# Optimization experiments

Measured on AMD Instinct MI355X. Metric: run time of the kernel, lower is better.

The kernel has to match this reference:

```python
import jax, jax.numpy as jnp
import numpy as np

NEG_SLOPE = 0.2  # PyG GATConv default negative_slope


def _gat_edge_forward(x, edge_index, edge_attr, W, W_edge, att_src, att_dst, att_edge, bias):
    N = x.shape[0]
    H, C = att_src.shape
    src, dst = edge_index[0], edge_index[1]

    # --- add self loops with edge_attr fill_value='mean' (PyG default) ---
    ones = jnp.ones((edge_attr.shape[0],), dtype=x.dtype)
    cnt = jax.ops.segment_sum(ones, dst, num_segments=N)  # [N]
    attr_sum = jax.ops.segment_sum(edge_attr, dst, num_segments=N)  # [N, edge_dim]
    loop_attr = attr_sum / jnp.maximum(cnt, 1.0)[:, None]  # mean, 0 if no in-edges
    loop_idx = jnp.arange(N, dtype=edge_index.dtype)
    src_all = jnp.concatenate([src, loop_idx])
    dst_all = jnp.concatenate([dst, loop_idx])
    attr_all = jnp.concatenate([edge_attr, loop_attr], axis=0)  # [E+N, edge_dim]

    # --- linear projections ---
    x_l = (x @ W).reshape(N, H, C)  # [N,H,C]; GATConv uses same lin for src/dst
    a_src = jnp.einsum('nhc,hc->nh', x_l, att_src)  # [N,H]
    a_dst = jnp.einsum('nhc,hc->nh', x_l, att_dst)  # [N,H]
    e = (attr_all @ W_edge).reshape(-1, H, C)  # [E+N,H,C]
    a_edge = jnp.einsum('ehc,hc->eh', e, att_edge)  # [E+N,H]

    # --- per-edge attention logits + segment softmax over incoming edges ---
    logits = jax.nn.leaky_relu(a_src[src_all] + a_dst[dst_all] + a_edge, NEG_SLOPE)
    m = jax.ops.segment_max(logits, dst_all, num_segments=N)  # [N,H]
    p = jnp.exp(logits - m[dst_all])
    denom = jax.ops.segment_sum(p, dst_all, num_segments=N)  # [N,H]
    alpha = p / denom[dst_all]  # [E+N,H]

    # --- weighted scatter aggregation ---
    msgs = alpha[:, :, None] * x_l[src_all]  # [E+N,H,C]
    out = jax.ops.segment_sum(msgs, dst_all, num_segments=N)  # [N,H,C]
    return out.reshape(N, H * C) + bias  # concat=True -> [N, H*C]


def setup_inputs() -> dict:
    key = jax.random.key(0)
    ks = jax.random.split(key, 8)
    N, E, DIN, EDIM, H, C = 100000, 1600000, 128, 16, 4, 32
    s = 1.0 / np.sqrt(DIN)
    return {
        'x': jax.random.normal(ks[0], (N, DIN), jnp.float32),
        'edge_index': jax.random.randint(ks[1], (2, E), 0, N, jnp.int64),
        'edge_attr': jax.random.normal(ks[2], (E, EDIM), jnp.float32),
        'W': jax.random.normal(ks[3], (DIN, H * C), jnp.float32) * s,
        'W_edge': jax.random.normal(ks[4], (EDIM, H * C), jnp.float32) * (1.0 / np.sqrt(EDIM)),
        'att_src': jax.random.normal(ks[5], (H, C), jnp.float32) * 0.1,
        'att_dst': jax.random.normal(ks[6], (H, C), jnp.float32) * 0.1,
        'att_edge': jax.random.normal(ks[7], (H, C), jnp.float32) * 0.1,
        'bias': jnp.zeros((H * C,), jnp.float32),
    }


def reference(x, edge_index, edge_attr, W, W_edge, att_src, att_dst, att_edge, bias):
    return _gat_edge_forward(x, edge_index, edge_attr, W, W_edge, att_src, att_dst, att_edge, bias)
```

## Files before the change

### kernel.cpp

```cpp
#include <hip/hip_runtime.h>
#include <hip/hip_fp16.h>
#include <math.h>

#define NEG_SLOPE 0.2f
typedef unsigned short ushort_t;
typedef unsigned int uint_t;

__global__ void k_prep(const int* __restrict__ ei, int* __restrict__ is64,
                       int* __restrict__ deg, int N,
                       const float* __restrict__ W_edge, const float* __restrict__ att_edge,
                       float* __restrict__ v_edge) {
  int b = blockIdx.x, t = threadIdx.x;
  if (b == 0) {
    __shared__ int any;
    if (t == 0) any = 0;
    __syncthreads();
    if (ei[2 * t + 1] != 0) atomicOr(&any, 1);
    __syncthreads();
    if (t == 0) *is64 = (any == 0) ? 1 : 0;
  } else if (b == 1) {
    if (t < 64) {
      int h = t >> 4, j = t & 15;
      float s = 0.f;
#pragma unroll
      for (int c = 0; c < 32; ++c) s += W_edge[j * 128 + h * 32 + c] * att_edge[h * 32 + c];
      v_edge[t] = s;
    }
  } else {
    int i = (b - 2) * 256 + t;
    if (i < N) deg[i] = 0;
  }
}

__global__ __launch_bounds__(256) void k1_xl(
    const float* __restrict__ x, const float* __restrict__ W,
    const float* __restrict__ att_src, const float* __restrict__ att_dst,
    ushort_t* __restrict__ x_l_h, float* __restrict__ a_src, float* __restrict__ a_dst, int N) {
  __shared__ float Wc[32 * 128];
  __shared__ float Xc[32 * 64];
  const int t = threadIdx.x;
  const int tcol = t & 31;
  const int trow = t >> 5;
  const int row0 = blockIdx.x * 64;
  const int r = t & 63, kq = t >> 6;
  const float4 aw_s = *(const float4*)&att_src[tcol * 4];
  const float4 aw_d = *(const float4*)&att_dst[tcol * 4];
  float acc[8][4];
#pragma unroll
  for (int i = 0; i < 8; ++i) { acc[i][0] = acc[i][1] = acc[i][2] = acc[i][3] = 0.f; }

  for (int kc = 0; kc < 4; ++kc) {
    float4 wreg[4];
#pragma unroll
    for (int q = 0; q < 4; ++q) wreg[q] = *(const float4*)&W[kc * 4096 + (q * 256 + t) * 4];
    float xs8[8];
    int grow = row0 + r;
    if (grow < N) {
      *(float4*)&xs8[0] = *(const float4*)&x[grow * 128 + kc * 32 + kq * 8];
      *(float4*)&xs8[4] = *(const float4*)&x[grow * 128 + kc * 32 + kq * 8 + 4];
    } else {
#pragma unroll
      for (int q = 0; q < 8; ++q) xs8[q] = 0.f;
    }
    __syncthreads();
#pragma unroll
    for (int q = 0; q < 4; ++q) *(float4*)&Wc[(q * 256 + t) * 4] = wreg[q];
#pragma unroll
    for (int q = 0; q < 8; ++q) Xc[(kq * 8 + q) * 64 + r] = xs8[q];
    __syncthreads();
#pragma unroll
    for (int kk = 0; kk < 32; ++kk) {
      float4 wv = *(const float4*)&Wc[kk * 128 + tcol * 4];
      float xr[8];
      *(float4*)&xr[0] = *(const float4*)&Xc[kk * 64 + trow * 8];
      *(float4*)&xr[4] = *(const float4*)&Xc[kk * 64 + trow * 8 + 4];
#pragma unroll
      for (int ri = 0; ri < 8; ++ri) {
        acc[ri][0] += xr[ri] * wv.x;
        acc[ri][1] += xr[ri] * wv.y;
        acc[ri][2] += xr[ri] * wv.z;
        acc[ri][3] += xr[ri] * wv.w;
      }
    }
  }
#pragma unroll
  for (int ri = 0; ri < 8; ++ri) {
    int grow = row0 + trow * 8 + ri;
    float asp = acc[ri][0] * aw_s.x + acc[ri][1] * aw_s.y + acc[ri][2] * aw_s.z + acc[ri][3] * aw_s.w;
    float adp = acc[ri][0] * aw_d.x + acc[ri][1] * aw_d.y + acc[ri][2] * aw_d.z + acc[ri][3] * aw_d.w;
#pragma unroll
    for (int m = 1; m < 8; m <<= 1) { asp += __shfl_xor(asp, m); adp += __shfl_xor(adp, m); }
    if (grow < N) {
      __half2 h0 = __floats2half2_rn(acc[ri][0], acc[ri][1]);
      __half2 h1 = __floats2half2_rn(acc[ri][2], acc[ri][3]);
      uint2 u; u.x = *(uint_t*)&h0; u.y = *(uint_t*)&h1;
      *(uint2*)&x_l_h[(size_t)grow * 128 + tcol * 4] = u;
      if ((tcol & 7) == 0) {
        a_src[grow * 4 + (tcol >> 3)] = asp;
        a_dst[grow * 4 + (tcol >> 3)] = adp;
      }
    }
  }
}

__global__ void k_hist(const int* __restrict__ ei, const int* __restrict__ is64,
                       int* __restrict__ deg, int* __restrict__ rank, int E) {
  int i = blockIdx.x * blockDim.x + threadIdx.x;
  if (i >= E) return;
  int dst = (*is64) ? ei[2 * (E + i)] : ei[E + i];
  rank[i] = atomicAdd(&deg[dst], 1);
}

__global__ void k_scan1(const int* __restrict__ deg, int* __restrict__ bsum, int N) {
  __shared__ int lds[256];
  int b = blockIdx.x, t = threadIdx.x;
  int base = b * 1024 + t * 4;
  int s = 0;
  if (base + 3 < N) {
    int4 v = *(const int4*)&deg[base];
    s = v.x + v.y + v.z + v.w;
  } else {
    for (int q = 0; q < 4; ++q) if (base + q < N) s += deg[base + q];
  }
  lds[t] = s; __syncthreads();
  for (int st = 128; st > 0; st >>= 1) {
    if (t < st) lds[t] += lds[t + st];
    __syncthreads();
  }
  if (t == 0) bsum[b] = lds[0];
}

__global__ void k_scan2(const int* __restrict__ bsum, int* __restrict__ boff, int NB) {
  __shared__ int lds[256];
  int t = threadIdx.x;
  int v = (t < NB) ? bsum[t] : 0;
  lds[t] = v;
  __syncthreads();
  for (int st = 1; st < 256; st <<= 1) {
    int add = (t >= st) ? lds[t - st] : 0;
    __syncthreads();
    lds[t] += add;
    __syncthreads();
  }
  if (t < NB) boff[t] = lds[t] - v;
}

__global__ void k_scan3(const int* __restrict__ deg, const int* __restrict__ boff,
                        int* __restrict__ offs, int N) {
  __shared__ int lds[256];
  int b = blockIdx.x, t = threadIdx.x;
  int base = b * 1024 + t * 4;
  int v[4]; int s = 0;
#pragma unroll
  for (int q = 0; q < 4; ++q) { v[q] = (base + q < N) ? deg[base + q] : 0; s += v[q]; }
  lds[t] = s;
  __syncthreads();
  for (int st = 1; st < 256; st <<= 1) {
    int add = (t >= st) ? lds[t - st] : 0;
    __syncthreads();
    lds[t] += add;
    __syncthreads();
  }
  int run = boff[b] + lds[t] - s;
#pragma unroll
  for (int q = 0; q < 4; ++q) {
    if (base + q < N) offs[base + q] = run;
    run += v[q];
  }
}

__global__ __launch_bounds__(256) void k_scatter(
    const int* __restrict__ ei, const int* __restrict__ is64,
    const int* __restrict__ rank, const int* __restrict__ offs,
    const float* __restrict__ edge_attr, const float* __restrict__ v_edge,
    int4* __restrict__ rec, int E) {
  __shared__ float ve[64];
  int t = threadIdx.x;
  if (t < 64) ve[t] = v_edge[t];
  __syncthreads();
  int i = blockIdx.x * 256 + t;
  if (i >= E) return;
  int f = *is64;
  int src = f ? ei[2 * i] : ei[i];
  int dst = f ? ei[2 * (E + i)] : ei[E + i];
  float a16[16];
  *(float4*)&a16[0]  = *(const float4*)&edge_attr[(size_t)i * 16];
  *(float4*)&a16[4]  = *(const float4*)&edge_attr[(size_t)i * 16 + 4];
  *(float4*)&a16[8]  = *(const float4*)&edge_attr[(size_t)i * 16 + 8];
  *(float4*)&a16[12] = *(const float4*)&edge_attr[(size_t)i * 16 + 12];
  float ae[4];
#pragma unroll
  for (int h = 0; h < 4; ++h) {
    float s = 0.f;
#pragma unroll
    for (int j = 0; j < 16; ++j) s += a16[j] * ve[h * 16 + j];
    ae[h] = s;
  }
  int pos = offs[dst] + rank[i];
  __half2 e01 = __floats2half2_rn(ae[0], ae[1]);
  __half2 e23 = __floats2half2_rn(ae[2], ae[3]);
  int4 r; r.x = *(int*)&e01; r.y = *(int*)&e23; r.z = src; r.w = 0;
  rec[pos] = r;
}

__global__ __launch_bounds__(256) void k34_agg(
    const int4* __restrict__ rec, const ushort_t* __restrict__ x_l_h,
    const float* __restrict__ a_src, const float* __restrict__ a_dst,
    const int* __restrict__ deg, const int* __restrict__ offs,
    const float* __restrict__ bias, float* __restrict__ out, int N) {
  int lane = threadIdx.x & 63;
  int node = blockIdx.x * 4 + (threadIdx.x >> 6);
  if (node >= N) return;
  int off = offs[node], dg = deg[node];
  int h = lane >> 4;
  float ad = a_dst[(size_t)node * 4 + h];
  const uint_t* xu = (const uint_t*)x_l_h;
  float accx = 0.f, accy = 0.f, den = 0.f, sae = 0.f;
  int i = 0;
  for (; i + 4 <= dg; i += 4) {
    int4 u0 = rec[off + i], u1 = rec[off + i + 1], u2 = rec[off + i + 2], u3 = rec[off + i + 3];
    uint_t v0 = xu[(size_t)u0.z * 64 + lane];
    uint_t v1 = xu[(size_t)u1.z * 64 + lane];
    uint_t v2 = xu[(size_t)u2.z * 64 + lane];
    uint_t v3 = xu[(size_t)u3.z * 64 + lane];
    float s0 = a_src[(size_t)u0.z * 4 + h];
    float s1 = a_src[(size_t)u1.z * 4 + h];
    float s2 = a_src[(size_t)u2.z * 4 + h];
    float s3 = a_src[(size_t)u3.z * 4 + h];
    uint_t w0 = (h & 2) ? (uint_t)u0.y : (uint_t)u0.x;
    uint_t w1 = (h & 2) ? (uint_t)u1.y : (uint_t)u1.x;
    uint_t w2 = (h & 2) ? (uint_t)u2.y : (uint_t)u2.x;
    uint_t w3 = (h & 2) ? (uint_t)u3.y : (uint_t)u3.x;
    float2 q0 = __half22float2(*(const __half2*)&w0);
    float2 q1 = __half22float2(*(const __half2*)&w1);
    float2 q2 = __half22float2(*(const __half2*)&w2);
    float2 q3 = __half22float2(*(const __half2*)&w3);
    float e0 = (h & 1) ? q0.y : q0.x;
    float e1 = (h & 1) ? q1.y : q1.x;
    float e2 = (h & 1) ? q2.y : q2.x;
    float e3 = (h & 1) ? q3.y : q3.x;
    float g0 = s0 + ad + e0; g0 = (g0 >= 0.f) ? g0 : NEG_SLOPE * g0;
    float g1 = s1 + ad + e1; g1 = (g1 >= 0.f) ? g1 : NEG_SLOPE * g1;
    float g2 = s2 + ad + e2; g2 = (g2 >= 0.f) ? g2 : NEG_SLOPE * g2;
    float g3 = s3 + ad + e3; g3 = (g3 >= 0.f) ? g3 : NEG_SLOPE * g3;
    float p0 = __expf(g0), p1 = __expf(g1), p2 = __expf(g2), p3 = __expf(g3);
    den += p0 + p1 + p2 + p3;
    sae += e0 + e1 + e2 + e3;
    float2 f0 = __half22float2(*(const __half2*)&v0);
    float2 f1 = __half22float2(*(const __half2*)&v1);
    float2 f2 = __half22float2(*(const __half2*)&v2);
    float2 f3 = __half22float2(*(const __half2*)&v3);
    accx += p0 * f0.x; accy += p0 * f0.y;
    accx += p1 * f1.x; accy += p1 * f1.y;
    accx += p2 * f2.x; accy += p2 * f2.y;
    accx += p3 * f3.x; accy += p3 * f3.y;
  }
  for (; i < dg; ++i) {
    int4 u = rec[off + i];
    uint_t v = xu[(size_t)u.z * 64 + lane];
    float as = a_src[(size_t)u.z * 4 + h];
    uint_t w = (h & 2) ? (uint_t)u.y : (uint_t)u.x;
    float2 q = __half22float2(*(const __half2*)&w);
    float ae = (h & 1) ? q.y : q.x;
    float g = as + ad + ae; g = (g >= 0.f) ? g : NEG_SLOPE * g;
    float p = __expf(g);
    den += p; sae += ae;
    float2 f = __half22float2(*(const __half2*)&v);
    accx += p * f.x; accy += p * f.y;
  }
  float as_n = a_src[(size_t)node * 4 + h];
  float inv_cnt = 1.f / (float)(dg > 0 ? dg : 1);
  float gl = as_n + ad + sae * inv_cnt;
  gl = (gl >= 0.f) ? gl : NEG_SLOPE * gl;
  float pl = __expf(gl);
  float iv = 1.f / (den + pl);
  uint_t vn = xu[(size_t)node * 64 + lane];
  float2 fn = __half22float2(*(const __half2*)&vn);
  float2 b2 = *(const float2*)&bias[2 * lane];
  float2 o;
  o.x = (accx + pl * fn.x) * iv + b2.x;
  o.y = (accy + pl * fn.y) * iv + b2.y;
  *(float2*)&out[(size_t)node * 128 + 2 * lane] = o;
}

extern "C" void kernel_launch(void* const* d_in, const int* in_sizes, int n_in,
                              void* d_out, int out_size, void* d_ws, size_t ws_size,
                              hipStream_t stream) {
  const float* x        = (const float*)d_in[0];
  const int*   ei       = (const int*)  d_in[1];
  const float* eattr    = (const float*)d_in[2];
  const float* W        = (const float*)d_in[3];
  const float* W_edge   = (const float*)d_in[4];
  const float* att_src  = (const float*)d_in[5];
  const float* att_dst  = (const float*)d_in[6];
  const float* att_edge = (const float*)d_in[7];
  const float* bias     = (const float*)d_in[8];
  float* out = (float*)d_out;
  const int N = in_sizes[0] / 128;
  const int E = in_sizes[1] / 2;
  (void)n_in; (void)out_size; (void)ws_size;

  char* base = (char*)d_ws;
  size_t off = 0;
  auto take = [&](size_t bytes) -> void* {
    void* p = base + off;
    off = (off + bytes + 255) & ~(size_t)255;
    return p;
  };
  ushort_t* x_l_h = (ushort_t*)take((size_t)N * 128 * 2);
  float* a_src    = (float*)take((size_t)N * 4 * 4);
  float* a_dst    = (float*)take((size_t)N * 4 * 4);
  float* v_edge   = (float*)take(64 * 4);
  int4*  rec      = (int4*)take((size_t)E * 16);
  int*   deg      = (int*)take((size_t)N * 4);
  int*   offs     = (int*)take((size_t)N * 4);
  int*   rank     = (int*)take((size_t)E * 4);
  int*   bsum     = (int*)take(256 * 4);
  int*   boff     = (int*)take(256 * 4);
  int*   is64     = (int*)take(4);

  const int NB = (N + 1023) / 1024;
  const int nbh = (E + 255) / 256;

  hipLaunchKernelGGL(k_prep, dim3(2 + (N + 255) / 256), dim3(256), 0, stream,
                     ei, is64, deg, N, W_edge, att_edge, v_edge);
  hipLaunchKernelGGL(k_hist, dim3(nbh), dim3(256), 0, stream, ei, is64, deg, rank, E);
  hipLaunchKernelGGL(k1_xl, dim3((N + 63) / 64), dim3(256), 0, stream,
                     x, W, att_src, att_dst, x_l_h, a_src, a_dst, N);
  hipLaunchKernelGGL(k_scan1, dim3(NB), dim3(256), 0, stream, deg, bsum, N);
  hipLaunchKernelGGL(k_scan2, dim3(1), dim3(256), 0, stream, bsum, boff, NB);
  hipLaunchKernelGGL(k_scan3, dim3(NB), dim3(256), 0, stream, deg, boff, offs, N);
  hipLaunchKernelGGL(k_scatter, dim3(nbh), dim3(256), 0, stream,
                     ei, is64, rank, offs, eattr, v_edge, rec, E);
  hipLaunchKernelGGL(k34_agg, dim3((N + 3) / 4), dim3(256), 0, stream,
                     rec, x_l_h, a_src, a_dst, deg, offs, bias, out, N);
}
```

Baseline: 295.1 us.

## Precompute unnormalized edge attention weights in scatter kernel, store fp8 edge logits

Moves the per-edge logit computation (a_src gather, leaky ReLU, exp) from the aggregation kernel into the scatter kernel. The scatter kernel now writes fp16 exp weights plus fp8-packed edge attention terms into the record, so aggregation skips the random a_src gathers and the exps. Source indices and offsets are made wave-uniform with readfirstlane so the x_l row addresses become scalar. The exp is taken without subtracting the segment max and the edge terms used for the self-loop mean are stored in fp8, which risks overflow and extra rounding error.

```diff
diff --git a/kernel.cpp b/kernel.cpp
--- a/kernel.cpp
+++ b/kernel.cpp
@@ -5,6 +5,46 @@
 #define NEG_SLOPE 0.2f
 typedef unsigned short ushort_t;
 typedef unsigned int uint_t;
+
+#if defined(__has_builtin)
+#if __has_builtin(__builtin_amdgcn_cvt_pk_fp8_f32) && __has_builtin(__builtin_amdgcn_cvt_f32_fp8)
+#define HAVE_FP8_CVT 1
+#endif
+#endif
+
+__device__ __forceinline__ uint_t pack_fp8x4(float a, float b, float c, float d) {
+#ifdef HAVE_FP8_CVT
+  int v = __builtin_amdgcn_cvt_pk_fp8_f32(a, b, 0, false);
+  v = __builtin_amdgcn_cvt_pk_fp8_f32(c, d, v, true);
+  return (uint_t)v;
+#else
+  auto enc = [](float x) -> uint_t {
+    uint_t bb = __float_as_uint(x);
+    uint_t s = (bb >> 24) & 0x80u;
+    int e = (int)((bb >> 23) & 0xffu);
+    uint_t m = (bb >> 20) & 7u;
+    m += (bb >> 19) & 1u;
+    if (m > 7u) { m = 0u; e++; }
+    e = e - 127 + 7;
+    if (e <= 0) return s;
+    if (e > 15) return s | 0x7eu;
+    return s | ((uint_t)e << 3) | m;
+  };
+  return enc(a) | (enc(b) << 8) | (enc(c) << 16) | (enc(d) << 24);
+#endif
+}
+
+__device__ __forceinline__ float unpack_fp8(uint_t w, int shift) {
+#ifdef HAVE_FP8_CVT
+  return __builtin_amdgcn_cvt_f32_fp8((int)(w >> shift), 0);
+#else
+  uint_t b = (w >> shift) & 0xffu;
+  uint_t s = (b & 0x80u) << 24;
+  uint_t em = b & 0x7fu;
+  uint_t f = s | ((em << 20) + (120u << 23));
+  return (em == 0u) ? __uint_as_float(s) : __uint_as_float(f);
+#endif
+}
 
 __global__ void k_prep(const int* __restrict__ ei, int* __restrict__ is64,
                        int* __restrict__ deg, int N,
@@ -173,6 +213,7 @@
     const int* __restrict__ ei, const int* __restrict__ is64,
     const int* __restrict__ rank, const int* __restrict__ offs,
     const float* __restrict__ edge_attr, const float* __restrict__ v_edge,
+    const float* __restrict__ a_src, const float* __restrict__ a_dst,
     int4* __restrict__ rec, int E) {
   __shared__ float ve[64];
   int t = threadIdx.x;
@@ -196,56 +237,62 @@
     for (int j = 0; j < 16; ++j) s += a16[j] * ve[h * 16 + j];
     ae[h] = s;
   }
+  float4 as4 = *(const float4*)&a_src[(size_t)src * 4];
+  float4 ad4 = *(const float4*)&a_dst[(size_t)dst * 4];
+  const float* asp = (const float*)&as4;
+  const float* adp = (const float*)&ad4;
+  float p[4];
+#pragma unroll
+  for (int h = 0; h < 4; ++h) {
+    float g = asp[h] + adp[h] + ae[h];
+    g = fmaxf(g, NEG_SLOPE * g);
+    p[h] = __expf(g);
+  }
+  __half2 p01 = __floats2half2_rn(p[0], p[1]);
+  __half2 p23 = __floats2half2_rn(p[2], p[3]);
+  uint_t aepk = pack_fp8x4(ae[0], ae[1], ae[2], ae[3]);
   int pos = offs[dst] + rank[i];
-  __half2 e01 = __floats2half2_rn(ae[0], ae[1]);
-  __half2 e23 = __floats2half2_rn(ae[2], ae[3]);
-  int4 r; r.x = *(int*)&e01; r.y = *(int*)&e23; r.z = src; r.w = 0;
+  int4 r; r.x = *(int*)&p01; r.y = *(int*)&p23; r.z = src; r.w = (int)aepk;
   rec[pos] = r;
 }
 
 __global__ __launch_bounds__(256) void k34_agg(
-    const int4* __restrict__ rec, const ushort_t* __restrict__ x_l_h,
+    const int4* __restrict__ rec, const uint_t* __restrict__ xu,
     const float* __restrict__ a_src, const float* __restrict__ a_dst,
     const int* __restrict__ deg, const int* __restrict__ offs,
     const float* __restrict__ bias, float* __restrict__ out, int N) {
   int lane = threadIdx.x & 63;
   int node = blockIdx.x * 4 + (threadIdx.x >> 6);
   if (node >= N) return;
-  int off = offs[node], dg = deg[node];
+  int offu = __builtin_amdgcn_readfirstlane(offs[node]);
+  int dgu  = __builtin_amdgcn_readfirstlane(deg[node]);
+  const int4* rp = rec + offu;
   int h = lane >> 4;
-  float ad = a_dst[(size_t)node * 4 + h];
-  const uint_t* xu = (const uint_t*)x_l_h;
+  int hs16 = (h & 1) << 4;
+  int hs8  = h << 3;
   float accx = 0.f, accy = 0.f, den = 0.f, sae = 0.f;
   int i = 0;
-  for (; i + 4 <= dg; i += 4) {
-    int4 u0 = rec[off + i], u1 = rec[off + i + 1], u2 = rec[off + i + 2], u3 = rec[off + i + 3];
-    uint_t v0 = xu[(size_t)u0.z * 64 + lane];
-    uint_t v1 = xu[(size_t)u1.z * 64 + lane];
-    uint_t v2 = xu[(size_t)u2.z * 64 + lane];
-    uint_t v3 = xu[(size_t)u3.z * 64 + lane];
-    float s0 = a_src[(size_t)u0.z * 4 + h];
-    float s1 = a_src[(size_t)u1.z * 4 + h];
-    float s2 = a_src[(size_t)u2.z * 4 + h];
-    float s3 = a_src[(size_t)u3.z * 4 + h];
+  for (; i + 4 <= dgu; i += 4) {
+    int4 u0 = rp[i], u1 = rp[i + 1], u2 = rp[i + 2], u3 = rp[i + 3];
+    int s0 = __builtin_amdgcn_readfirstlane(u0.z);
+    int s1 = __builtin_amdgcn_readfirstlane(u1.z);
+    int s2 = __builtin_amdgcn_readfirstlane(u2.z);
+    int s3 = __builtin_amdgcn_readfirstlane(u3.z);
+    uint_t v0 = xu[((size_t)(uint_t)s0 << 6) + lane];
+    uint_t v1 = xu[((size_t)(uint_t)s1 << 6) + lane];
+    uint_t v2 = xu[((size_t)(uint_t)s2 << 6) + lane];
+    uint_t v3 = xu[((size_t)(uint_t)s3 << 6) + lane];
     uint_t w0 = (h & 2) ? (uint_t)u0.y : (uint_t)u0.x;
     uint_t w1 = (h & 2) ? (uint_t)u1.y : (uint_t)u1.x;
     uint_t w2 = (h & 2) ? (uint_t)u2.y : (uint_t)u2.x;
     uint_t w3 = (h & 2) ? (uint_t)u3.y : (uint_t)u3.x;
-    float2 q0 = __half22float2(*(const __half2*)&w0);
-    float2 q1 = __half22float2(*(const __half2*)&w1);
-    float2 q2 = __half22float2(*(const __half2*)&w2);
-    float2 q3 = __half22float2(*(const __half2*)&w3);
-    float e0 = (h & 1) ? q0.y : q0.x;
-    float e1 = (h & 1) ? q1.y : q1.x;
-    float e2 = (h & 1) ? q2.y : q2.x;
-    float e3 = (h & 1) ? q3.y : q3.x;
-    float g0 = s0 + ad + e0; g0 = (g0 >= 0.f) ? g0 : NEG_SLOPE * g0;
-    float g1 = s1 + ad + e1; g1 = (g1 >= 0.f) ? g1 : NEG_SLOPE * g1;
-    float g2 = s2 + ad + e2; g2 = (g2 >= 0.f) ? g2 : NEG_SLOPE * g2;
-    float g3 = s3 + ad + e3; g3 = (g3 >= 0.f) ? g3 : NEG_SLOPE * g3;
-    float p0 = __expf(g0), p1 = __expf(g1), p2 = __expf(g2), p3 = __expf(g3);
+    float p0 = __half2float(__ushort_as_half((ushort_t)(w0 >> hs16)));
+    float p1 = __half2float(__ushort_as_half((ushort_t)(w1 >> hs16)));
+    float p2 = __half2float(__ushort_as_half((ushort_t)(w2 >> hs16)));
+    float p3 = __half2float(__ushort_as_half((ushort_t)(w3 >> hs16)));
     den += p0 + p1 + p2 + p3;
-    sae += e0 + e1 + e2 + e3;
+    sae += unpack_fp8((uint_t)u0.w, hs8) + unpack_fp8((uint_t)u1.w, hs8)
+         + unpack_fp8((uint_t)u2.w, hs8) + unpack_fp8((uint_t)u3.w, hs8);
     float2 f0 = __half22float2(*(const __half2*)&v0);
     float2 f1 = __half22float2(*(const __half2*)&v1);
     float2 f2 = __half22float2(*(const __half2*)&v2);
@@ -255,26 +302,25 @@
     accx += p2 * f2.x; accy += p2 * f2.y;
     accx += p3 * f3.x; accy += p3 * f3.y;
   }
-  for (; i < dg; ++i) {
-    int4 u = rec[off + i];
-    uint_t v = xu[(size_t)u.z * 64 + lane];
-    float as = a_src[(size_t)u.z * 4 + h];
+  for (; i < dgu; ++i) {
+    int4 u = rp[i];
+    int s = __builtin_amdgcn_readfirstlane(u.z);
+    uint_t v = xu[((size_t)(uint_t)s << 6) + lane];
     uint_t w = (h & 2) ? (uint_t)u.y : (uint_t)u.x;
-    float2 q = __half22float2(*(const __half2*)&w);
-    float ae = (h & 1) ? q.y : q.x;
-    float g = as + ad + ae; g = (g >= 0.f) ? g : NEG_SLOPE * g;
-    float p = __expf(g);
-    den += p; sae += ae;
-    float2 f = __half22float2(*(const __half2*)&v);
-    accx += p * f.x; accy += p * f.y;
-  }
-  float as_n = a_src[(size_t)node * 4 + h];
-  float inv_cnt = 1.f / (float)(dg > 0 ? dg : 1);
-  float gl = as_n + ad + sae * inv_cnt;
-  gl = (gl >= 0.f) ? gl : NEG_SLOPE * gl;
+    float p = __half2float(__ushort_as_half((ushort_t)(w >> hs16)));
+    den += p;
+    sae += unpack_fp8((uint_t)u.w, hs8);
+    float2 fx = __half22float2(*(const __half2*)&v);
+    accx += p * fx.x; accy += p * fx.y;
+  }
+  float ad  = a_dst[(size_t)node * 4 + h];
+  float asn = a_src[(size_t)node * 4 + h];
+  float inv_cnt = 1.f / (float)(dgu > 0 ? dgu : 1);
+  float gl = asn + ad + sae * inv_cnt;
+  gl = fmaxf(gl, NEG_SLOPE * gl);
   float pl = __expf(gl);
   float iv = 1.f / (den + pl);
-  uint_t vn = xu[(size_t)node * 64 + lane];
+  uint_t vn = xu[((size_t)(uint_t)node << 6) + lane];
   float2 fn = __half22float2(*(const __half2*)&vn);
   float2 b2 = *(const float2*)&bias[2 * lane];
   float2 o;
@@ -331,7 +377,7 @@
   hipLaunchKernelGGL(k_scan2, dim3(1), dim3(256), 0, stream, bsum, boff, NB);
   hipLaunchKernelGGL(k_scan3, dim3(NB), dim3(256), 0, stream, deg, boff, offs, N);
   hipLaunchKernelGGL(k_scatter, dim3(nbh), dim3(256), 0, stream,
-                     ei, is64, rank, offs, eattr, v_edge, rec, E);
+                     ei, is64, rank, offs, eattr, v_edge, a_src, a_dst, rec, E);
   hipLaunchKernelGGL(k34_agg, dim3((N + 3) / 4), dim3(256), 0, stream,
-                     rec, x_l_h, a_src, a_dst, deg, offs, bias, out, N);
-}
+                     rec, (const uint_t*)x_l_h, a_src, a_dst, deg, offs, bias, out, N);
+}
```

New measurement: 296.9 us. About the same (+0.6%).

## Fuse node projection GEMM with edge scatter into one launch; scalarize agg indices

Applied to the files above, without the earlier changes.

Merges the x@W projection kernel and the edge scatter kernel into a single launch. Scatter blocks come first and the GEMM blocks follow, so the compute-bound GEMM overlaps with the memory-bound scatter instead of running alone. The aggregation kernel now uses readfirstlane to keep offsets, degrees and source indices in scalar registers, and uses fmax for leaky relu and a shift for half extraction. The fused kernel reserves the GEMM's LDS for scatter blocks too, which may lower their occupancy.

```diff
diff --git a/kernel.cpp b/kernel.cpp
--- a/kernel.cpp
+++ b/kernel.cpp
@@ -32,16 +32,114 @@
   }
 }
 
-__global__ __launch_bounds__(256) void k1_xl(
+__global__ void k_hist(const int* __restrict__ ei, const int* __restrict__ is64,
+                       int* __restrict__ deg, int* __restrict__ rank, int E) {
+  int i = blockIdx.x * blockDim.x + threadIdx.x;
+  if (i >= E) return;
+  int dst = (*is64) ? ei[2 * (E + i)] : ei[E + i];
+  rank[i] = atomicAdd(&deg[dst], 1);
+}
+
+__global__ void k_scan1(const int* __restrict__ deg, int* __restrict__ bsum, int N) {
+  __shared__ int lds[256];
+  int b = blockIdx.x, t = threadIdx.x;
+  int base = b * 1024 + t * 4;
+  int s = 0;
+  if (base + 3 < N) {
+    int4 v = *(const int4*)&deg[base];
+    s = v.x + v.y + v.z + v.w;
+  } else {
+    for (int q = 0; q < 4; ++q) if (base + q < N) s += deg[base + q];
+  }
+  lds[t] = s; __syncthreads();
+  for (int st = 128; st > 0; st >>= 1) {
+    if (t < st) lds[t] += lds[t + st];
+    __syncthreads();
+  }
+  if (t == 0) bsum[b] = lds[0];
+}
+
+__global__ void k_scan2(const int* __restrict__ bsum, int* __restrict__ boff, int NB) {
+  __shared__ int lds[256];
+  int t = threadIdx.x;
+  int v = (t < NB) ? bsum[t] : 0;
+  lds[t] = v;
+  __syncthreads();
+  for (int st = 1; st < 256; st <<= 1) {
+    int add = (t >= st) ? lds[t - st] : 0;
+    __syncthreads();
+    lds[t] += add;
+    __syncthreads();
+  }
+  if (t < NB) boff[t] = lds[t] - v;
+}
+
+__global__ void k_scan3(const int* __restrict__ deg, const int* __restrict__ boff,
+                        int* __restrict__ offs, int N) {
+  __shared__ int lds[256];
+  int b = blockIdx.x, t = threadIdx.x;
+  int base = b * 1024 + t * 4;
+  int v[4]; int s = 0;
+#pragma unroll
+  for (int q = 0; q < 4; ++q) { v[q] = (base + q < N) ? deg[base + q] : 0; s += v[q]; }
+  lds[t] = s;
+  __syncthreads();
+  for (int st = 1; st < 256; st <<= 1) {
+    int add = (t >= st) ? lds[t - st] : 0;
+    __syncthreads();
+    lds[t] += add;
+    __syncthreads();
+  }
+  int run = boff[b] + lds[t] - s;
+#pragma unroll
+  for (int q = 0; q < 4; ++q) {
+    if (base + q < N) offs[base + q] = run;
+    run += v[q];
+  }
+}
+
+__global__ __launch_bounds__(256) void k1_scatter(
     const float* __restrict__ x, const float* __restrict__ W,
     const float* __restrict__ att_src, const float* __restrict__ att_dst,
-    ushort_t* __restrict__ x_l_h, float* __restrict__ a_src, float* __restrict__ a_dst, int N) {
+    ushort_t* __restrict__ x_l_h, float* __restrict__ a_src, float* __restrict__ a_dst, int N,
+    const int* __restrict__ ei, const int* __restrict__ is64,
+    const int* __restrict__ rank, const int* __restrict__ offs,
+    const float* __restrict__ edge_attr, const float* __restrict__ v_edge,
+    int4* __restrict__ rec, int E, int nbs) {
   __shared__ float Wc[32 * 128];
   __shared__ float Xc[32 * 64];
   const int t = threadIdx.x;
+  if (blockIdx.x < nbs) {
+    if (t < 64) Wc[t] = v_edge[t];
+    __syncthreads();
+    int i = blockIdx.x * 256 + t;
+    if (i >= E) return;
+    int f = *is64;
+    int src = f ? ei[2 * i] : ei[i];
+    int dst = f ? ei[2 * (E + i)] : ei[E + i];
+    float a16[16];
+    *(float4*)&a16[0]  = *(const float4*)&edge_attr[(size_t)i * 16];
+    *(float4*)&a16[4]  = *(const float4*)&edge_attr[(size_t)i * 16 + 4];
+    *(float4*)&a16[8]  = *(const float4*)&edge_attr[(size_t)i * 16 + 8];
+    *(float4*)&a16[12] = *(const float4*)&edge_attr[(size_t)i * 16 + 12];
+    float ae[4];
+#pragma unroll
+    for (int h = 0; h < 4; ++h) {
+      float s = 0.f;
+#pragma unroll
+      for (int j = 0; j < 16; ++j) s += a16[j] * Wc[h * 16 + j];
+      ae[h] = s;
+    }
+    int pos = offs[dst] + rank[i];
+    __half2 e01 = __floats2half2_rn(ae[0], ae[1]);
+    __half2 e23 = __floats2half2_rn(ae[2], ae[3]);
+    int4 r; r.x = *(int*)&e01; r.y = *(int*)&e23; r.z = src; r.w = 0;
+    rec[pos] = r;
+    return;
+  }
   const int tcol = t & 31;
   const int trow = t >> 5;
-  const int row0 = blockIdx.x * 64;
+  const int row0 = (blockIdx.x - nbs) * 64;
   const int r = t & 63, kq = t >> 6;
   const float4 aw_s = *(const float4*)&att_src[tcol * 4];
   const float4 aw_d = *(const float4*)&att_dst[tcol * 4];
@@ -103,146 +201,48 @@
   }
 }
 
-__global__ void k_hist(const int* __restrict__ ei, const int* __restrict__ is64,
-                       int* __restrict__ deg, int* __restrict__ rank, int E) {
-  int i = blockIdx.x * blockDim.x + threadIdx.x;
-  if (i >= E) return;
-  int dst = (*is64) ? ei[2 * (E + i)] : ei[E + i];
-  rank[i] = atomicAdd(&deg[dst], 1);
-}
-
-__global__ void k_scan1(const int* __restrict__ deg, int* __restrict__ bsum, int N) {
-  __shared__ int lds[256];
-  int b = blockIdx.x, t = threadIdx.x;
-  int base = b * 1024 + t * 4;
-  int s = 0;
-  if (base + 3 < N) {
-    int4 v = *(const int4*)&deg[base];
-    s = v.x + v.y + v.z + v.w;
-  } else {
-    for (int q = 0; q < 4; ++q) if (base + q < N) s += deg[base + q];
-  }
-  lds[t] = s; __syncthreads();
-  for (int st = 128; st > 0; st >>= 1) {
-    if (t < st) lds[t] += lds[t + st];
-    __syncthreads();
-  }
-  if (t == 0) bsum[b] = lds[0];
-}
-
-__global__ void k_scan2(const int* __restrict__ bsum, int* __restrict__ boff, int NB) {
-  __shared__ int lds[256];
-  int t = threadIdx.x;
-  int v = (t < NB) ? bsum[t] : 0;
-  lds[t] = v;
-  __syncthreads();
-  for (int st = 1; st < 256; st <<= 1) {
-    int add = (t >= st) ? lds[t - st] : 0;
-    __syncthreads();
-    lds[t] += add;
-    __syncthreads();
-  }
-  if (t < NB) boff[t] = lds[t] - v;
-}
-
-__global__ void k_scan3(const int* __restrict__ deg, const int* __restrict__ boff,
-                        int* __restrict__ offs, int N) {
-  __shared__ int lds[256];
-  int b = blockIdx.x, t = threadIdx.x;
-  int base = b * 1024 + t * 4;
-  int v[4]; int s = 0;
-#pragma unroll
-  for (int q = 0; q < 4; ++q) { v[q] = (base + q < N) ? deg[base + q] : 0; s += v[q]; }
-  lds[t] = s;
-  __syncthreads();
-  for (int st = 1; st < 256; st <<= 1) {
-    int add = (t >= st) ? lds[t - st] : 0;
-    __syncthreads();
-    lds[t] += add;
-    __syncthreads();
-  }
-  int run = boff[b] + lds[t] - s;
-#pragma unroll
-  for (int q = 0; q < 4; ++q) {
-    if (base + q < N) offs[base + q] = run;
-    run += v[q];
-  }
-}
-
-__global__ __launch_bounds__(256) void k_scatter(
-    const int* __restrict__ ei, const int* __restrict__ is64,
-    const int* __restrict__ rank, const int* __restrict__ offs,
-    const float* __restrict__ edge_attr, const float* __restrict__ v_edge,
-    int4* __restrict__ rec, int E) {
-  __shared__ float ve[64];
-  int t = threadIdx.x;
-  if (t < 64) ve[t] = v_edge[t];
-  __syncthreads();
-  int i = blockIdx.x * 256 + t;
-  if (i >= E) return;
-  int f = *is64;
-  int src = f ? ei[2 * i] : ei[i];
-  int dst = f ? ei[2 * (E + i)] : ei[E + i];
-  float a16[16];
-  *(float4*)&a16[0]  = *(const float4*)&edge_attr[(size_t)i * 16];
-  *(float4*)&a16[4]  = *(const float4*)&edge_attr[(size_t)i * 16 + 4];
-  *(float4*)&a16[8]  = *(const float4*)&edge_attr[(size_t)i * 16 + 8];
-  *(float4*)&a16[12] = *(const float4*)&edge_attr[(size_t)i * 16 + 12];
-  float ae[4];
-#pragma unroll
-  for (int h = 0; h < 4; ++h) {
-    float s = 0.f;
-#pragma unroll
-    for (int j = 0; j < 16; ++j) s += a16[j] * ve[h * 16 + j];
-    ae[h] = s;
-  }
-  int pos = offs[dst] + rank[i];
-  __half2 e01 = __floats2half2_rn(ae[0], ae[1]);
-  __half2 e23 = __floats2half2_rn(ae[2], ae[3]);
-  int4 r; r.x = *(int*)&e01; r.y = *(int*)&e23; r.z = src; r.w = 0;
-  rec[pos] = r;
-}
-
 __global__ __launch_bounds__(256) void k34_agg(
-    const int4* __restrict__ rec, const ushort_t* __restrict__ x_l_h,
+    const int4* __restrict__ rec, const uint_t* __restrict__ xu,
     const float* __restrict__ a_src, const float* __restrict__ a_dst,
     const int* __restrict__ deg, const int* __restrict__ offs,
     const float* __restrict__ bias, float* __restrict__ out, int N) {
   int lane = threadIdx.x & 63;
   int node = blockIdx.x * 4 + (threadIdx.x >> 6);
   if (node >= N) return;
-  int off = offs[node], dg = deg[node];
+  int offu = __builtin_amdgcn_readfirstlane(offs[node]);
+  int dgu  = __builtin_amdgcn_readfirstlane(deg[node]);
+  const int4* rp = rec + offu;
   int h = lane >> 4;
+  int hs16 = (h & 1) << 4;
   float ad = a_dst[(size_t)node * 4 + h];
-  const uint_t* xu = (const uint_t*)x_l_h;
   float accx = 0.f, accy = 0.f, den = 0.f, sae = 0.f;
   int i = 0;
-  for (; i + 4 <= dg; i += 4) {
-    int4 u0 = rec[off + i], u1 = rec[off + i + 1], u2 = rec[off + i + 2], u3 = rec[off + i + 3];
-    uint_t v0 = xu[(size_t)u0.z * 64 + lane];
-    uint_t v1 = xu[(size_t)u1.z * 64 + lane];
-    uint_t v2 = xu[(size_t)u2.z * 64 + lane];
-    uint_t v3 = xu[(size_t)u3.z * 64 + lane];
-    float s0 = a_src[(size_t)u0.z * 4 + h];
-    float s1 = a_src[(size_t)u1.z * 4 + h];
-    float s2 = a_src[(size_t)u2.z * 4 + h];
-    float s3 = a_src[(size_t)u3.z * 4 + h];
+  for (; i + 4 <= dgu; i += 4) {
+    int4 u0 = rp[i], u1 = rp[i + 1], u2 = rp[i + 2], u3 = rp[i + 3];
+    int s0 = __builtin_amdgcn_readfirstlane(u0.z);
+    int s1 = __builtin_amdgcn_readfirstlane(u1.z);
+    int s2 = __builtin_amdgcn_readfirstlane(u2.z);
+    int s3 = __builtin_amdgcn_readfirstlane(u3.z);
+    uint_t v0 = xu[((size_t)(uint_t)s0 << 6) + lane];
+    uint_t v1 = xu[((size_t)(uint_t)s1 << 6) + lane];
+    uint_t v2 = xu[((size_t)(uint_t)s2 << 6) + lane];
+    uint_t v3 = xu[((size_t)(uint_t)s3 << 6) + lane];
+    float as0 = a_src[((size_t)(uint_t)s0 << 2) + h];
+    float as1 = a_src[((size_t)(uint_t)s1 << 2) + h];
+    float as2 = a_src[((size_t)(uint_t)s2 << 2) + h];
+    float as3 = a_src[((size_t)(uint_t)s3 << 2) + h];
     uint_t w0 = (h & 2) ? (uint_t)u0.y : (uint_t)u0.x;
     uint_t w1 = (h & 2) ? (uint_t)u1.y : (uint_t)u1.x;
     uint_t w2 = (h & 2) ? (uint_t)u2.y : (uint_t)u2.x;
     uint_t w3 = (h & 2) ? (uint_t)u3.y : (uint_t)u3.x;
-    float2 q0 = __half22float2(*(const __half2*)&w0);
-    float2 q1 = __half22float2(*(const __half2*)&w1);
-    float2 q2 = __half22float2(*(const __half2*)&w2);
-    float2 q3 = __half22float2(*(const __half2*)&w3);
-    float e0 = (h & 1) ? q0.y : q0.x;
-    float e1 = (h & 1) ? q1.y : q1.x;
-    float e2 = (h & 1) ? q2.y : q2.x;
-    float e3 = (h & 1) ? q3.y : q3.x;
-    float g0 = s0 + ad + e0; g0 = (g0 >= 0.f) ? g0 : NEG_SLOPE * g0;
-    float g1 = s1 + ad + e1; g1 = (g1 >= 0.f) ? g1 : NEG_SLOPE * g1;
-    float g2 = s2 + ad + e2; g2 = (g2 >= 0.f) ? g2 : NEG_SLOPE * g2;
-    float g3 = s3 + ad + e3; g3 = (g3 >= 0.f) ? g3 : NEG_SLOPE * g3;
+    float e0 = __half2float(__ushort_as_half((ushort_t)(w0 >> hs16)));
+    float e1 = __half2float(__ushort_as_half((ushort_t)(w1 >> hs16)));
+    float e2 = __half2float(__ushort_as_half((ushort_t)(w2 >> hs16)));
+    float e3 = __half2float(__ushort_as_half((ushort_t)(w3 >> hs16)));
+    float g0 = as0 + ad + e0; g0 = fmaxf(g0, NEG_SLOPE * g0);
+    float g1 = as1 + ad + e1; g1 = fmaxf(g1, NEG_SLOPE * g1);
+    float g2 = as2 + ad + e2; g2 = fmaxf(g2, NEG_SLOPE * g2);
+    float g3 = as3 + ad + e3; g3 = fmaxf(g3, NEG_SLOPE * g3);
     float p0 = __expf(g0), p1 = __expf(g1), p2 = __expf(g2), p3 = __expf(g3);
     den += p0 + p1 + p2 + p3;
     sae += e0 + e1 + e2 + e3;
@@ -255,26 +255,26 @@
     accx += p2 * f2.x; accy += p2 * f2.y;
     accx += p3 * f3.x; accy += p3 * f3.y;
   }
-  for (; i < dg; ++i) {
-    int4 u = rec[off + i];
-    uint_t v = xu[(size_t)u.z * 64 + lane];
-    float as = a_src[(size_t)u.z * 4 + h];
+  for (; i < dgu; ++i) {
+    int4 u = rp[i];
+    int s = __builtin_amdgcn_readfirstlane(u.z);
+    uint_t v = xu[((size_t)(uint_t)s << 6) + lane];
+    float as = a_src[((size_t)(uint_t)s << 2) + h];
     uint_t w = (h & 2) ? (uint_t)u.y : (uint_t)u.x;
-    float2 q = __half22float2(*(const __half2*)&w);
-    float ae = (h & 1) ? q.y : q.x;
-    float g = as + ad + ae; g = (g >= 0.f) ? g : NEG_SLOPE * g;
+    float e = __half2float(__ushort_as_half((ushort_t)(w >> hs16)));
+    float g = as + ad + e; g = fmaxf(g, NEG_SLOPE * g);
     float p = __expf(g);
-    den += p; sae += ae;
-    float2 f = __half22float2(*(const __half2*)&v);
-    accx += p * f.x; accy += p * f.y;
-  }
-  float as_n = a_src[(size_t)node * 4 + h];
-  float inv_cnt = 1.f / (float)(dg > 0 ? dg : 1);
-  float gl = as_n + ad + sae * inv_cnt;
-  gl = (gl >= 0.f) ? gl : NEG_SLOPE * gl;
+    den += p; sae += e;
+    float2 fx = __half22float2(*(const __half2*)&v);
+    accx += p * fx.x; accy += p * fx.y;
+  }
+  float asn = a_src[(size_t)node * 4 + h];
+  float inv_cnt = 1.f / (float)(dgu > 0 ? dgu : 1);
+  float gl = asn + ad + sae * inv_cnt;
+  gl = fmaxf(gl, NEG_SLOPE * gl);
   float pl = __expf(gl);
   float iv = 1.f / (den + pl);
-  uint_t vn = xu[(size_t)node * 64 + lane];
+  uint_t vn = xu[((size_t)(uint_t)node << 6) + lane];
   float2 fn = __half22float2(*(const __half2*)&vn);
   float2 b2 = *(const float2*)&bias[2 * lane];
   float2 o;
@@ -320,18 +320,18 @@
   int*   is64     = (int*)take(4);
 
   const int NB = (N + 1023) / 1024;
-  const int nbh = (E + 255) / 256;
+  const int nbs = (E + 255) / 256;
+  const int nb1 = (N + 63) / 64;
 
   hipLaunchKernelGGL(k_prep, dim3(2 + (N + 255) / 256), dim3(256), 0, stream,
                      ei, is64, deg, N, W_edge, att_edge, v_edge);
-  hipLaunchKernelGGL(k_hist, dim3(nbh), dim3(256), 0, stream, ei, is64, deg, rank, E);
-  hipLaunchKernelGGL(k1_xl, dim3((N + 63) / 64), dim3(256), 0, stream,
-                     x, W, att_src, att_dst, x_l_h, a_src, a_dst, N);
+  hipLaunchKernelGGL(k_hist, dim3(nbs), dim3(256), 0, stream, ei, is64, deg, rank, E);
   hipLaunchKernelGGL(k_scan1, dim3(NB), dim3(256), 0, stream, deg, bsum, N);
   hipLaunchKernelGGL(k_scan2, dim3(1), dim3(256), 0, stream, bsum, boff, NB);
   hipLaunchKernelGGL(k_scan3, dim3(NB), dim3(256), 0, stream, deg, boff, offs, N);
-  hipLaunchKernelGGL(k_scatter, dim3(nbh), dim3(256), 0, stream,
-                     ei, is64, rank, offs, eattr, v_edge, rec, E);
+  hipLaunchKernelGGL(k1_scatter, dim3(nbs + nb1), dim3(256), 0, stream,
+                     x, W, att_src, att_dst, x_l_h, a_src, a_dst, N,
+                     ei, is64, rank, offs, eattr, v_edge, rec, E, nbs);
   hipLaunchKernelGGL(k34_agg, dim3((N + 3) / 4), dim3(256), 0, stream,
-                     rec, x_l_h, a_src, a_dst, deg, offs, bias, out, N);
-}
+                     rec, (const uint_t*)x_l_h, a_src, a_dst, deg, offs, bias, out, N);
+}
```

Measured after the change: 267.8 us. 9.3% less time.
